# Performance work log

Hardware: AMD Instinct MI355X
Metric: run time of the kernel (lower is better)

## Reference

```python
import jax, jax.numpy as jnp
import numpy as np

DIM = 64        # feature channels of x
HEADS = 4
POS_DIM = 3
NUM_IDS = 8
STR_IN = 512    # strength_linear input size
B, S, W = 4, 1024, 8   # batch, sequence (S1), source-views (S2)


def setup_inputs() -> dict:
    key = jax.random.key(0)
    ks = jax.random.split(key, 18)
    stdv = 1.0 / np.sqrt(DIM * DIM)  # embedding init per module
    d8 = DIM // 8
    u = lambda k, shp, s: jax.random.uniform(k, shp, jnp.float32, -s, s)
    return {
        "x": jax.random.normal(ks[0], (B, DIM, S, W), jnp.float32),
        "pos": jax.random.normal(ks[1], (B, S, POS_DIM), jnp.float32),
        "strength": jax.random.normal(ks[2], (STR_IN,), jnp.float32),
        "embed_id1": 3,
        "q_emb_w": u(ks[3], (NUM_IDS, DIM * DIM), stdv),
        "k_emb_w": u(ks[4], (NUM_IDS, DIM * DIM), stdv),
        "v_emb_w": u(ks[5], (NUM_IDS, DIM * DIM), stdv),
        "pos_w1": u(ks[6], (POS_DIM, POS_DIM), 1.0 / np.sqrt(POS_DIM)),
        "pos_b1": u(ks[7], (POS_DIM,), 1.0 / np.sqrt(POS_DIM)),
        "pos_w2": u(ks[8], (d8, POS_DIM), 1.0 / np.sqrt(POS_DIM)),
        "pos_b2": u(ks[9], (d8,), 1.0 / np.sqrt(POS_DIM)),
        "head_w": u(ks[10], (HEADS, d8), 1.0 / np.sqrt(d8)),
        "head_b": u(ks[11], (HEADS,), 1.0 / np.sqrt(d8)),
        "gate": jnp.ones((HEADS,), jnp.float32),
        "out_w": u(ks[12], (DIM, DIM), 1.0 / np.sqrt(DIM)),
        "out_b": u(ks[13], (DIM,), 1.0 / np.sqrt(DIM)),
        "str_w": u(ks[14], (DIM, STR_IN), 1.0 / np.sqrt(STR_IN)),
        "str_b": u(ks[15], (DIM,), 1.0 / np.sqrt(STR_IN)),
    }


def reference(x, pos, strength, embed_id1, q_emb_w, k_emb_w, v_emb_w,
              pos_w1, pos_b1, pos_w2, pos_b2, head_w, head_b, gate,
              out_w, out_b, str_w, str_b):
    # strength projection: Linear(512, dim)
    s = strength @ str_w.T + str_b                    # [dim]
    xt = jnp.transpose(x, (0, 2, 3, 1))               # [B, S, W, dim]
    qe = q_emb_w[embed_id1].reshape(DIM, DIM)
    ke = k_emb_w[embed_id1].reshape(DIM, DIM)
    ve = v_emb_w[embed_id1].reshape(DIM, DIM)

    def proj(emb):
        y = xt @ emb.T + s                            # [B, S, W, dim]
        # collapse (W, dim) -> (heads, head_dim), heads to axis 1
        y = y.reshape(B, S, HEADS, -1)
        return jnp.transpose(y, (0, 2, 1, 3))         # [B, H, S, hd]

    q, k, v = proj(qe), proj(ke), proj(ve)
    hd = q.shape[-1]
    attn = jax.nn.softmax(jnp.einsum("bhsd,bhtd->bhst", q, k) / np.sqrt(hd), axis=-1)

    # relative-position attention branch
    ph = jax.nn.relu(pos @ pos_w1.T + pos_b1) @ pos_w2.T + pos_b2   # [B, S, dim//8]
    diff = ph[:, :, None, :] - ph[:, None, :, :]                    # [B, S, S, dim//8]
    pos_attn = jnp.transpose(diff @ head_w.T + head_b, (0, 3, 1, 2))
    pos_attn = jax.nn.softmax(pos_attn, axis=-1)                    # [B, H, S, S]

    g = jax.nn.sigmoid(gate).reshape(1, -1, 1, 1)
    attn = (1.0 - g) * attn + g * pos_attn
    attn = attn / jnp.sum(attn, axis=-1, keepdims=True)

    out = jnp.einsum("bhst,bhtd->bhsd", attn, v)      # [B, H, S, hd]
    out = jnp.transpose(out, (0, 2, 1, 3)).reshape(B, S, W, DIM)
    return out @ out_w.T + out_b                      # [B, S, W, dim]
```

## Files before the change

kernel.cpp:

```cpp
#include <hip/hip_runtime.h>
#include <math.h>
#include <stdint.h>

#define B_ 4
#define S_ 1024
#define F_ 512
#define HD 128
#define SOFT_C 4.0f

typedef __attribute__((ext_vector_type(8))) short short8;
typedef __attribute__((ext_vector_type(4))) float f32x4;
typedef __attribute__((ext_vector_type(4))) unsigned int u32x4;
typedef __attribute__((ext_vector_type(2))) unsigned int u32x2;

__device__ __forceinline__ unsigned short f2bf(float f) {
    unsigned int u = __float_as_uint(f);
    u = (u + 0x7FFFu + ((u >> 16) & 1u)) >> 16;
    return (unsigned short)u;
}
__device__ __forceinline__ float bf2f(unsigned int s) {
    return __uint_as_float(s << 16);
}
__device__ __forceinline__ void pack_hilo(const float* v, u32x4& hi, u32x4& lo) {
    #pragma unroll
    for (int p = 0; p < 4; ++p) {
        unsigned int h0 = f2bf(v[2 * p]), h1 = f2bf(v[2 * p + 1]);
        float l0 = v[2 * p] - bf2f(h0), l1 = v[2 * p + 1] - bf2f(h1);
        hi[p] = h0 | (h1 << 16);
        lo[p] = (unsigned int)f2bf(l0) | ((unsigned int)f2bf(l1) << 16);
    }
}

__global__ __launch_bounds__(256) void k_prep(
    const int* __restrict__ embed_id,
    const float* __restrict__ qw, const float* __restrict__ kw,
    const float* __restrict__ vw, const float* __restrict__ ow,
    const float* __restrict__ pos,
    const float* __restrict__ pw1, const float* __restrict__ pb1,
    const float* __restrict__ pw2, const float* __restrict__ pb2,
    const float* __restrict__ head_w,
    const float* __restrict__ strength, const float* __restrict__ str_w,
    const float* __restrict__ str_b,
    unsigned short* __restrict__ packs,
    float* __restrict__ sv, float* __restrict__ svq,
    float* __restrict__ p_g)
{
    __shared__ float red_s[4][4];
    __shared__ float inv_s[4];
    const int blk = blockIdx.x, tid = threadIdx.x;
    const float SCALE = 0.08838834764831845f;

    if (blk < 4) {
        const int id = embed_id[0];
        const float* src = (blk == 0 ? qw + id * 4096 : blk == 1 ? kw + id * 4096
                            : blk == 2 ? vw + id * 4096 : ow);
        const float scale = (blk == 0) ? SCALE : 1.0f;
        unsigned short* hi = packs + blk * 8192;
        unsigned short* lo = hi + 4096;
        for (int i = tid; i < 4096; i += 256) {
            float v = src[i] * scale;
            unsigned short h = f2bf(v);
            hi[i] = h;
            lo[i] = f2bf(v - bf2f(h));
        }
    } else if (blk < 8) {
        const int b = blk - 4;
        const int wv = tid >> 6;
        float w1_[9], b1_[3], w2_[24], b2_[8], hw_[32];
        #pragma unroll
        for (int i = 0; i < 9; ++i)  w1_[i] = pw1[i];
        #pragma unroll
        for (int i = 0; i < 3; ++i)  b1_[i] = pb1[i];
        #pragma unroll
        for (int i = 0; i < 24; ++i) w2_[i] = pw2[i];
        #pragma unroll
        for (int i = 0; i < 8; ++i)  b2_[i] = pb2[i];
        #pragma unroll
        for (int i = 0; i < 32; ++i) hw_[i] = head_w[i];

        float ev[4][4];
        float ps[4] = {0.f, 0.f, 0.f, 0.f};
        #pragma unroll
        for (int k = 0; k < 4; ++k) {
            const int t = k * 256 + tid;
            float p0 = pos[(b * S_ + t) * 3 + 0];
            float p1 = pos[(b * S_ + t) * 3 + 1];
            float p2 = pos[(b * S_ + t) * 3 + 2];
            float h0 = fmaxf(0.f, p0 * w1_[0] + p1 * w1_[1] + p2 * w1_[2] + b1_[0]);
            float h1 = fmaxf(0.f, p0 * w1_[3] + p1 * w1_[4] + p2 * w1_[5] + b1_[1]);
            float h2 = fmaxf(0.f, p0 * w1_[6] + p1 * w1_[7] + p2 * w1_[8] + b1_[2]);
            float ph[8];
            #pragma unroll
            for (int o8 = 0; o8 < 8; ++o8)
                ph[o8] = h0 * w2_[o8 * 3] + h1 * w2_[o8 * 3 + 1] + h2 * w2_[o8 * 3 + 2] + b2_[o8];
            #pragma unroll
            for (int h = 0; h < 4; ++h) {
                float A = 0.f;
                #pragma unroll
                for (int o8 = 0; o8 < 8; ++o8) A += ph[o8] * hw_[h * 8 + o8];
                ev[k][h] = __expf(-A - 1.0f);
                ps[h] += ev[k][h];
            }
        }
        #pragma unroll
        for (int h = 0; h < 4; ++h)
            #pragma unroll
            for (int off = 1; off < 64; off <<= 1)
                ps[h] += __shfl_xor(ps[h], off);
        if ((tid & 63) == 0)
            #pragma unroll
            for (int h = 0; h < 4; ++h) red_s[wv][h] = ps[h];
        __syncthreads();
        if (tid < 4)
            inv_s[tid] = 1.f / (red_s[0][tid] + red_s[1][tid] + red_s[2][tid] + red_s[3][tid]);
        __syncthreads();
        #pragma unroll
        for (int k = 0; k < 4; ++k)
            #pragma unroll
            for (int h = 0; h < 4; ++h)
                p_g[(b * 4 + h) * S_ + k * 256 + tid] = ev[k][h] * inv_s[h];
    } else {
        __shared__ float part_s[4][64];
        const int c = tid & 63, pr = tid >> 6;
        const float* wrow = str_w + c * 512 + pr * 128;
        const float* st   = strength + pr * 128;
        float acc = 0.f;
        #pragma unroll
        for (int j4 = 0; j4 < 32; ++j4) {
            f32x4 wv4 = *(const f32x4*)(wrow + j4 * 4);
            f32x4 s4  = *(const f32x4*)(st + j4 * 4);
            acc += wv4[0] * s4[0] + wv4[1] * s4[1] + wv4[2] * s4[2] + wv4[3] * s4[3];
        }
        part_s[pr][c] = acc;
        __syncthreads();
        if (tid < 64) {
            float v = part_s[0][tid] + part_s[1][tid] + part_s[2][tid]
                    + part_s[3][tid] + str_b[tid];
            sv[tid] = v;
            svq[tid] = v * SCALE;
        }
    }
}

__global__ __launch_bounds__(256) void k_qkv(
    const float* __restrict__ x,
    const unsigned short* __restrict__ packs,
    const float* __restrict__ sv, const float* __restrict__ svq,
    const float* __restrict__ p_g,
    unsigned short* __restrict__ yqh, unsigned short* __restrict__ ykh,
    unsigned short* __restrict__ yvt2, float* __restrict__ xbar)
{
    __shared__ float xr_s[4][8];
    const int tid  = threadIdx.x;
    const int wv   = tid >> 6;
    const int lane = tid & 63;
    const int quad = lane >> 4;
    const int l15  = lane & 15;

    if (blockIdx.x >= 512) {
        const int bi = blockIdx.x - 512;
        const int b = bi >> 6, c = bi & 63;
        const float* xc = x + (size_t)b * 524288 + c * 8192;
        const float* pb = p_g + b * 4096;
        float acc[8] = {};
        #pragma unroll
        for (int rr = 0; rr < 4; ++rr) {
            const int s = tid * 4 + rr;
            f32x4 x0 = *(const f32x4*)(xc + s * 8);
            f32x4 x1 = *(const f32x4*)(xc + s * 8 + 4);
            float p0 = pb[s], p1 = pb[1024 + s], p2 = pb[2048 + s], p3 = pb[3072 + s];
            acc[0] += p0 * x0[0]; acc[1] += p0 * x0[1];
            acc[2] += p1 * x0[2]; acc[3] += p1 * x0[3];
            acc[4] += p2 * x1[0]; acc[5] += p2 * x1[1];
            acc[6] += p3 * x1[2]; acc[7] += p3 * x1[3];
        }
        #pragma unroll
        for (int j = 0; j < 8; ++j)
            #pragma unroll
            for (int off = 1; off < 64; off <<= 1)
                acc[j] += __shfl_xor(acc[j], off);
        if (lane == 0)
            #pragma unroll
            for (int j = 0; j < 8; ++j) xr_s[wv][j] = acc[j];
        __syncthreads();
        if (tid < 8)
            xbar[(b * 8 + tid) * 64 + c] = xr_s[0][tid] + xr_s[1][tid]
                                         + xr_s[2][tid] + xr_s[3][tid];
        return;
    }

    const int r0   = blockIdx.x * 64 + wv * 16;
    const int b    = r0 >> 13;
    const int rloc = (r0 & 8191) + l15;
    const float* xb = x + (size_t)b * 524288;

    u32x4 xhi[2], xlo[2];
    #pragma unroll
    for (int kc = 0; kc < 2; ++kc) {
        float xv[8];
        #pragma unroll
        for (int j = 0; j < 8; ++j)
            xv[j] = xb[(kc * 32 + quad * 8 + j) * 8192 + rloc];
        pack_hilo(xv, xhi[kc], xlo[kc]);
    }

    float svq_l[4], sv_l[4];
    #pragma unroll
    for (int nt = 0; nt < 4; ++nt) {
        svq_l[nt] = svq[nt * 16 + l15];
        sv_l[nt]  = sv[nt * 16 + l15];
    }
    f32x4 svA[4];
    #pragma unroll
    for (int mt = 0; mt < 4; ++mt)
        svA[mt] = *(const f32x4*)(sv + mt * 16 + quad * 4);

    int idxq[4];
    #pragma unroll
    for (int rr = 0; rr < 4; ++rr) {
        const int rl = quad * 4 + rr;
        const int w_ = rl & 7;
        const int s_loc = ((r0 & 8191) >> 3) + (rl >> 3);
        idxq[rr] = (b * 4 + (w_ >> 1)) * 131072 + s_loc * 128 + (w_ & 1) * 64 + l15;
    }

    const int row_g = r0 + l15;
    const int s_idx = (row_g >> 3) & 1023;
    const int w_idx = row_g & 7;
    const int bh    = b * 4 + (w_idx >> 1);
    const int dbase = (w_idx & 1) * 64;
    unsigned short* vtb = yvt2 + (size_t)bh * 131072 + (s_idx >> 6) * 8192
                        + (size_t)dbase * 64 + (s_idx & 63);

    #pragma unroll
    for (int mat = 0; mat < 2; ++mat) {
        const unsigned short* mh = packs + mat * 8192;
        const unsigned short* ml = mh + 4096;
        f32x4 acc[4] = {};
        #pragma unroll
        for (int kc = 0; kc < 2; ++kc)
            #pragma unroll
            for (int nt = 0; nt < 4; ++nt) {
                const int off = (nt * 16 + l15) * 64 + kc * 32 + quad * 8;
                u32x4 ehi = *(const u32x4*)(mh + off);
                u32x4 elo = *(const u32x4*)(ml + off);
                acc[nt] = __builtin_amdgcn_mfma_f32_16x16x32_bf16(
                    __builtin_bit_cast(short8, xhi[kc]),
                    __builtin_bit_cast(short8, ehi), acc[nt], 0, 0, 0);
                acc[nt] = __builtin_amdgcn_mfma_f32_16x16x32_bf16(
                    __builtin_bit_cast(short8, xlo[kc]),
                    __builtin_bit_cast(short8, ehi), acc[nt], 0, 0, 0);
                acc[nt] = __builtin_amdgcn_mfma_f32_16x16x32_bf16(
                    __builtin_bit_cast(short8, xhi[kc]),
                    __builtin_bit_cast(short8, elo), acc[nt], 0, 0, 0);
            }
        unsigned short* y = (mat == 0 ? yqh : ykh);
        const float* svp = (mat == 0 ? svq_l : sv_l);
        #pragma unroll
        for (int nt = 0; nt < 4; ++nt)
            #pragma unroll
            for (int rr = 0; rr < 4; ++rr)
                y[(size_t)idxq[rr] + nt * 16] = f2bf(acc[nt][rr] + svp[nt]);
    }

    {
        const unsigned short* mh = packs + 2 * 8192;
        const unsigned short* ml = mh + 4096;
        f32x4 acc[4] = {};
        #pragma unroll
        for (int kc = 0; kc < 2; ++kc)
            #pragma unroll
            for (int mt = 0; mt < 4; ++mt) {
                const int off = (mt * 16 + l15) * 64 + kc * 32 + quad * 8;
                u32x4 ehi = *(const u32x4*)(mh + off);
                u32x4 elo = *(const u32x4*)(ml + off);
                acc[mt] = __builtin_amdgcn_mfma_f32_16x16x32_bf16(
                    __builtin_bit_cast(short8, ehi),
                    __builtin_bit_cast(short8, xhi[kc]), acc[mt], 0, 0, 0);
                acc[mt] = __builtin_amdgcn_mfma_f32_16x16x32_bf16(
                    __builtin_bit_cast(short8, ehi),
                    __builtin_bit_cast(short8, xlo[kc]), acc[mt], 0, 0, 0);
                acc[mt] = __builtin_amdgcn_mfma_f32_16x16x32_bf16(
                    __builtin_bit_cast(short8, elo),
                    __builtin_bit_cast(short8, xhi[kc]), acc[mt], 0, 0, 0);
            }
        #pragma unroll
        for (int mt = 0; mt < 4; ++mt)
            #pragma unroll
            for (int rr = 0; rr < 4; ++rr) {
                const int c = mt * 16 + quad * 4 + rr;
                vtb[(size_t)c * 64] = f2bf(acc[mt][rr] + svA[mt][rr]);
            }
    }
}

__global__ __launch_bounds__(256, 2) void k_attn(
    const unsigned short* __restrict__ yqh, const unsigned short* __restrict__ ykh,
    const unsigned short* __restrict__ yvt2,
    const float* __restrict__ xbar, const float* __restrict__ vw,
    const int* __restrict__ embed_id, const float* __restrict__ sv,
    const float* __restrict__ gate, float* __restrict__ out)
{
    __shared__ __align__(16) unsigned short kx[2][64 * 136];
    __shared__ __align__(16) unsigned short vx[2][128 * 72];
    __shared__ float vbar_s[128];

    const int tid  = threadIdx.x;
    const int w    = tid >> 6;
    const int lane = tid & 63;
    const int quad = lane >> 4;
    const int l15  = lane & 15;
    const int bh = blockIdx.x & 15, qt = blockIdx.x >> 4;
    const int b = bh >> 2, h = bh & 3;
    const int s0 = qt * 32;
    const int qh = w >> 1;
    const int dh = w & 1;

    const unsigned short* ykb = ykh + (size_t)bh * 131072;
    const unsigned short* yvb = yvt2 + (size_t)bh * 131072;

    if (tid < 128) {
        const int c = tid & 63, wloc = tid >> 6;
        const float* ver = vw + embed_id[0] * 4096 + c * 64;
        const float* xbr = xbar + (b * 8 + h * 2 + wloc) * 64;
        float a = sv[c];
        #pragma unroll
        for (int j4 = 0; j4 < 16; ++j4) {
            f32x4 e4 = *(const f32x4*)(ver + j4 * 4);
            f32x4 x4 = *(const f32x4*)(xbr + j4 * 4);
            a += e4[0] * x4[0] + e4[1] * x4[1] + e4[2] * x4[2] + e4[3] * x4[3];
        }
        vbar_s[wloc * 64 + c] = a;
    }

    u32x4 qf[4];
    #pragma unroll
    for (int kc = 0; kc < 4; ++kc)
        qf[kc] = *(const u32x4*)(yqh + (size_t)bh * 131072
                 + (s0 + qh * 16 + l15) * 128 + kc * 32 + quad * 8);

    #pragma unroll
    for (int r = 0; r < 4; ++r) {
        const int off = r * 2048 + tid * 8;
        *(u32x4*)&kx[0][(off >> 7) * 136 + (off & 127)] =
            *(const u32x4*)(ykb + off);
        *(u32x4*)&vx[0][(off >> 6) * 72 + (off & 63)] =
            *(const u32x4*)(yvb + off);
    }
    __syncthreads();

    f32x4 o[4] = {};
    float lsum = 0.f;
    const int srcA = ((quad & 1) << 5) + l15;

    for (int it = 0; it < 16; ++it) {
        const int cur = it & 1;
        u32x4 kst[4], vst[4];
        const bool pre = (it < 15);
        if (pre) {
            const unsigned short* ksrc = ykb + (it + 1) * 8192;
            const unsigned short* vsrc = yvb + (it + 1) * 8192;
            #pragma unroll
            for (int r = 0; r < 4; ++r)
                kst[r] = *(const u32x4*)(ksrc + r * 2048 + tid * 8);
            #pragma unroll
            for (int r = 0; r < 4; ++r)
                vst[r] = *(const u32x4*)(vsrc + r * 2048 + tid * 8);
        }

        const unsigned short* kxc = kx[cur];
        const unsigned short* vxc = vx[cur];

        #pragma unroll
        for (int th = 0; th < 2; ++th) {
            f32x4 sa0 = {}, sa1 = {};
            #pragma unroll
            for (int kc = 0; kc < 4; ++kc) {
                u32x4 a0 = *(const u32x4*)&kxc[(th * 32 + l15) * 136 + kc * 32 + quad * 8];
                sa0 = __builtin_amdgcn_mfma_f32_16x16x32_bf16(
                    __builtin_bit_cast(short8, a0),
                    __builtin_bit_cast(short8, qf[kc]), sa0, 0, 0, 0);
            }
            #pragma unroll
            for (int kc = 0; kc < 4; ++kc) {
                u32x4 a1 = *(const u32x4*)&kxc[(th * 32 + 16 + l15) * 136 + kc * 32 + quad * 8];
                sa1 = __builtin_amdgcn_mfma_f32_16x16x32_bf16(
                    __builtin_bit_cast(short8, a1),
                    __builtin_bit_cast(short8, qf[kc]), sa1, 0, 0, 0);
            }

            float p0[4], p1[4];
            #pragma unroll
            for (int r = 0; r < 4; ++r) {
                p0[r] = __expf(sa0[r] - SOFT_C);
                p1[r] = __expf(sa1[r] - SOFT_C);
                lsum += p0[r] + p1[r];
            }

            unsigned int pk00 = (unsigned int)f2bf(p0[0]) | ((unsigned int)f2bf(p0[1]) << 16);
            unsigned int pk01 = (unsigned int)f2bf(p0[2]) | ((unsigned int)f2bf(p0[3]) << 16);
            unsigned int pk10 = (unsigned int)f2bf(p1[0]) | ((unsigned int)f2bf(p1[1]) << 16);
            unsigned int pk11 = (unsigned int)f2bf(p1[2]) | ((unsigned int)f2bf(p1[3]) << 16);
            unsigned int sel0 = (quad < 2) ? pk00 : pk10;
            unsigned int sel1 = (quad < 2) ? pk01 : pk11;
            u32x4 pf;
            pf[0] = (unsigned int)__shfl((int)sel0, srcA);
            pf[1] = (unsigned int)__shfl((int)sel1, srcA);
            pf[2] = (unsigned int)__shfl((int)sel0, srcA + 16);
            pf[3] = (unsigned int)__shfl((int)sel1, srcA + 16);

            #pragma unroll
            for (int dt = 0; dt < 4; ++dt) {
                u32x4 vf = *(const u32x4*)&vxc[(dh * 64 + dt * 16 + l15) * 72
                                               + th * 32 + quad * 8];
                o[dt] = __builtin_amdgcn_mfma_f32_16x16x32_bf16(
                    __builtin_bit_cast(short8, vf),
                    __builtin_bit_cast(short8, pf), o[dt], 0, 0, 0);
            }
        }

        if (pre) {
            #pragma unroll
            for (int r = 0; r < 4; ++r) {
                const int off = r * 2048 + tid * 8;
                *(u32x4*)&kx[cur ^ 1][(off >> 7) * 136 + (off & 127)] = kst[r];
            }
            #pragma unroll
            for (int r = 0; r < 4; ++r) {
                const int off = r * 2048 + tid * 8;
                *(u32x4*)&vx[cur ^ 1][(off >> 6) * 72 + (off & 63)] = vst[r];
            }
        }
        __syncthreads();
    }

    lsum += __shfl_xor(lsum, 16);
    lsum += __shfl_xor(lsum, 32);
    const float gf = 1.f / (1.f + __expf(-gate[h]));
    const float cf = (1.f - gf) / lsum;
    const int row = b * S_ + s0 + qh * 16 + l15;
    #pragma unroll
    for (int dt = 0; dt < 4; ++dt) {
        const int d0 = dh * 64 + dt * 16 + quad * 4;
        f32x4 vb = *(const f32x4*)&vbar_s[d0];
        f32x4 rv;
        #pragma unroll
        for (int j = 0; j < 4; ++j) rv[j] = cf * o[dt][j] + gf * vb[j];
        *(f32x4*)(out + (size_t)row * F_ + h * HD + d0) = rv;
    }
}

__global__ __launch_bounds__(256) void k_oproj(
    float* __restrict__ out, const unsigned short* __restrict__ packs,
    const float* __restrict__ ob)
{
    const int tid  = threadIdx.x;
    const int wv   = tid >> 6;
    const int lane = tid & 63;
    const int quad = lane >> 4;
    const int l15  = lane & 15;
    const int r0   = blockIdx.x * 64 + wv * 16;
    const unsigned short* owh = packs + 3 * 8192;
    const unsigned short* owl = owh + 4096;

    u32x4 bhi[2], blo[2];
    #pragma unroll
    for (int kc = 0; kc < 2; ++kc) {
        const float* src = out + (size_t)(r0 + l15) * 64 + kc * 32 + quad * 8;
        f32x4 y0 = *(const f32x4*)src;
        f32x4 y1 = *(const f32x4*)(src + 4);
        float yv8[8] = {y0[0], y0[1], y0[2], y0[3], y1[0], y1[1], y1[2], y1[3]};
        pack_hilo(yv8, bhi[kc], blo[kc]);
    }

    f32x4 acc[4] = {};
    #pragma unroll
    for (int kc = 0; kc < 2; ++kc)
        #pragma unroll
        for (int mt = 0; mt < 4; ++mt) {
            const int off = (mt * 16 + l15) * 64 + kc * 32 + quad * 8;
            u32x4 ahi = *(const u32x4*)(owh + off);
            u32x4 alo = *(const u32x4*)(owl + off);
            acc[mt] = __builtin_amdgcn_mfma_f32_16x16x32_bf16(
                __builtin_bit_cast(short8, ahi),
                __builtin_bit_cast(short8, bhi[kc]), acc[mt], 0, 0, 0);
            acc[mt] = __builtin_amdgcn_mfma_f32_16x16x32_bf16(
                __builtin_bit_cast(short8, ahi),
                __builtin_bit_cast(short8, blo[kc]), acc[mt], 0, 0, 0);
            acc[mt] = __builtin_amdgcn_mfma_f32_16x16x32_bf16(
                __builtin_bit_cast(short8, alo),
                __builtin_bit_cast(short8, bhi[kc]), acc[mt], 0, 0, 0);
        }

    #pragma unroll
    for (int mt = 0; mt < 4; ++mt) {
        f32x4 bias = *(const f32x4*)(ob + mt * 16 + quad * 4);
        f32x4 v = acc[mt] + bias;
        *(f32x4*)(out + (size_t)(r0 + l15) * 64 + mt * 16 + quad * 4) = v;
    }
}

extern "C" void kernel_launch(void* const* d_in, const int* in_sizes, int n_in,
                              void* d_out, int out_size, void* d_ws, size_t ws_size,
                              hipStream_t stream) {
    (void)in_sizes; (void)n_in; (void)out_size; (void)ws_size;
    const float* x        = (const float*)d_in[0];
    const float* pos      = (const float*)d_in[1];
    const float* strength = (const float*)d_in[2];
    const int*   embed_id = (const int*)d_in[3];
    const float* qw       = (const float*)d_in[4];
    const float* kw       = (const float*)d_in[5];
    const float* vw       = (const float*)d_in[6];
    const float* pw1      = (const float*)d_in[7];
    const float* pb1      = (const float*)d_in[8];
    const float* pw2      = (const float*)d_in[9];
    const float* pb2      = (const float*)d_in[10];
    const float* head_w   = (const float*)d_in[11];
    const float* gate     = (const float*)d_in[13];
    const float* out_w    = (const float*)d_in[14];
    const float* out_b    = (const float*)d_in[15];
    const float* str_w    = (const float*)d_in[16];
    const float* str_b    = (const float*)d_in[17];
    float* out = (float*)d_out;

    unsigned short* yqh   = (unsigned short*)d_ws;
    unsigned short* ykh   = yqh + 2097152;
    unsigned short* yvt2  = ykh + 2097152;
    unsigned short* packs = yvt2 + 2097152;
    float* sv   = (float*)(packs + 8 * 4096);
    float* svq  = sv + 64;
    float* p_g  = svq + 64;
    float* xbar = p_g + 16384;

    k_prep<<<9, 256, 0, stream>>>(embed_id, qw, kw, vw, out_w, pos,
                                  pw1, pb1, pw2, pb2, head_w,
                                  strength, str_w, str_b, packs, sv, svq, p_g);
    k_qkv<<<768, 256, 0, stream>>>(x, packs, sv, svq, p_g, yqh, ykh, yvt2, xbar);
    k_attn<<<512, 256, 0, stream>>>(yqh, ykh, yvt2, xbar, vw, embed_id, sv,
                                    gate, out);
    k_oproj<<<512, 256, 0, stream>>>(out, packs, out_b);
}
```

Before: 159.9 us.

## Fuse prep into QKV kernel and output projection into attention epilogue

The separate prep kernel is removed. Each QKV block now recomputes the strength projection and the hi/lo bf16 split of the Q/K/V weights into shared memory, in a swizzled layout. The xbar blocks recompute the position softmax themselves. The output-projection kernel is folded into the attention epilogue: partial outputs are reduced through shared memory, projected with out_w split on the fly, and the gated vbar term is pre-projected. The intent is to remove two launches and a global round trip of the attention output, at the cost of redundant per-block weight conversion and larger shared memory use that may lower occupancy.

```diff
diff --git a/kernel.cpp b/kernel.cpp
--- a/kernel.cpp
+++ b/kernel.cpp
@@ -31,148 +31,103 @@
     }
 }
 
-__global__ __launch_bounds__(256) void k_prep(
-    const int* __restrict__ embed_id,
+__global__ __launch_bounds__(256) void k_qkv(
+    const float* __restrict__ x, const int* __restrict__ embed_id,
     const float* __restrict__ qw, const float* __restrict__ kw,
-    const float* __restrict__ vw, const float* __restrict__ ow,
-    const float* __restrict__ pos,
-    const float* __restrict__ pw1, const float* __restrict__ pb1,
-    const float* __restrict__ pw2, const float* __restrict__ pb2,
-    const float* __restrict__ head_w,
+    const float* __restrict__ vw,
     const float* __restrict__ strength, const float* __restrict__ str_w,
     const float* __restrict__ str_b,
-    unsigned short* __restrict__ packs,
-    float* __restrict__ sv, float* __restrict__ svq,
-    float* __restrict__ p_g)
+    const float* __restrict__ pos, const float* __restrict__ pw1,
+    const float* __restrict__ pb1, const float* __restrict__ pw2,
+    const float* __restrict__ pb2, const float* __restrict__ head_w,
+    unsigned short* __restrict__ yqh, unsigned short* __restrict__ ykh,
+    unsigned short* __restrict__ yvt2,
+    float* __restrict__ sv_g, float* __restrict__ xbar)
 {
+    __shared__ unsigned short whi[3][4096];
+    __shared__ unsigned short wlo[3][4096];
+    __shared__ float part_s[4][64];
+    __shared__ float sv_s[64], svq_s[64];
+    __shared__ float xr_s[4][8];
     __shared__ float red_s[4][4];
     __shared__ float inv_s[4];
-    const int blk = blockIdx.x, tid = threadIdx.x;
-    const float SCALE = 0.08838834764831845f;
-
-    if (blk < 4) {
-        const int id = embed_id[0];
-        const float* src = (blk == 0 ? qw + id * 4096 : blk == 1 ? kw + id * 4096
-                            : blk == 2 ? vw + id * 4096 : ow);
-        const float scale = (blk == 0) ? SCALE : 1.0f;
-        unsigned short* hi = packs + blk * 8192;
-        unsigned short* lo = hi + 4096;
-        for (int i = tid; i < 4096; i += 256) {
-            float v = src[i] * scale;
-            unsigned short h = f2bf(v);
-            hi[i] = h;
-            lo[i] = f2bf(v - bf2f(h));
-        }
-    } else if (blk < 8) {
-        const int b = blk - 4;
-        const int wv = tid >> 6;
-        float w1_[9], b1_[3], w2_[24], b2_[8], hw_[32];
-        #pragma unroll
-        for (int i = 0; i < 9; ++i)  w1_[i] = pw1[i];
-        #pragma unroll
-        for (int i = 0; i < 3; ++i)  b1_[i] = pb1[i];
-        #pragma unroll
-        for (int i = 0; i < 24; ++i) w2_[i] = pw2[i];
-        #pragma unroll
-        for (int i = 0; i < 8; ++i)  b2_[i] = pb2[i];
-        #pragma unroll
-        for (int i = 0; i < 32; ++i) hw_[i] = head_w[i];
-
-        float ev[4][4];
-        float ps[4] = {0.f, 0.f, 0.f, 0.f};
-        #pragma unroll
-        for (int k = 0; k < 4; ++k) {
-            const int t = k * 256 + tid;
-            float p0 = pos[(b * S_ + t) * 3 + 0];
-            float p1 = pos[(b * S_ + t) * 3 + 1];
-            float p2 = pos[(b * S_ + t) * 3 + 2];
-            float h0 = fmaxf(0.f, p0 * w1_[0] + p1 * w1_[1] + p2 * w1_[2] + b1_[0]);
-            float h1 = fmaxf(0.f, p0 * w1_[3] + p1 * w1_[4] + p2 * w1_[5] + b1_[1]);
-            float h2 = fmaxf(0.f, p0 * w1_[6] + p1 * w1_[7] + p2 * w1_[8] + b1_[2]);
-            float ph[8];
-            #pragma unroll
-            for (int o8 = 0; o8 < 8; ++o8)
-                ph[o8] = h0 * w2_[o8 * 3] + h1 * w2_[o8 * 3 + 1] + h2 * w2_[o8 * 3 + 2] + b2_[o8];
-            #pragma unroll
-            for (int h = 0; h < 4; ++h) {
-                float A = 0.f;
-                #pragma unroll
-                for (int o8 = 0; o8 < 8; ++o8) A += ph[o8] * hw_[h * 8 + o8];
-                ev[k][h] = __expf(-A - 1.0f);
-                ps[h] += ev[k][h];
-            }
-        }
-        #pragma unroll
-        for (int h = 0; h < 4; ++h)
-            #pragma unroll
-            for (int off = 1; off < 64; off <<= 1)
-                ps[h] += __shfl_xor(ps[h], off);
-        if ((tid & 63) == 0)
-            #pragma unroll
-            for (int h = 0; h < 4; ++h) red_s[wv][h] = ps[h];
-        __syncthreads();
-        if (tid < 4)
-            inv_s[tid] = 1.f / (red_s[0][tid] + red_s[1][tid] + red_s[2][tid] + red_s[3][tid]);
-        __syncthreads();
-        #pragma unroll
-        for (int k = 0; k < 4; ++k)
-            #pragma unroll
-            for (int h = 0; h < 4; ++h)
-                p_g[(b * 4 + h) * S_ + k * 256 + tid] = ev[k][h] * inv_s[h];
-    } else {
-        __shared__ float part_s[4][64];
-        const int c = tid & 63, pr = tid >> 6;
-        const float* wrow = str_w + c * 512 + pr * 128;
-        const float* st   = strength + pr * 128;
-        float acc = 0.f;
-        #pragma unroll
-        for (int j4 = 0; j4 < 32; ++j4) {
-            f32x4 wv4 = *(const f32x4*)(wrow + j4 * 4);
-            f32x4 s4  = *(const f32x4*)(st + j4 * 4);
-            acc += wv4[0] * s4[0] + wv4[1] * s4[1] + wv4[2] * s4[2] + wv4[3] * s4[3];
-        }
-        part_s[pr][c] = acc;
-        __syncthreads();
-        if (tid < 64) {
-            float v = part_s[0][tid] + part_s[1][tid] + part_s[2][tid]
-                    + part_s[3][tid] + str_b[tid];
-            sv[tid] = v;
-            svq[tid] = v * SCALE;
-        }
-    }
-}
-
-__global__ __launch_bounds__(256) void k_qkv(
-    const float* __restrict__ x,
-    const unsigned short* __restrict__ packs,
-    const float* __restrict__ sv, const float* __restrict__ svq,
-    const float* __restrict__ p_g,
-    unsigned short* __restrict__ yqh, unsigned short* __restrict__ ykh,
-    unsigned short* __restrict__ yvt2, float* __restrict__ xbar)
-{
-    __shared__ float xr_s[4][8];
+
     const int tid  = threadIdx.x;
     const int wv   = tid >> 6;
     const int lane = tid & 63;
     const int quad = lane >> 4;
     const int l15  = lane & 15;
+    const float SCALE = 0.08838834764831845f;
 
     if (blockIdx.x >= 512) {
         const int bi = blockIdx.x - 512;
         const int b = bi >> 6, c = bi & 63;
+        float w1_[9], b1_[3], w2_[24], b2_[8], hw_[32];
+        #pragma unroll
+        for (int i = 0; i < 9; ++i)  w1_[i] = pw1[i];
+        #pragma unroll
+        for (int i = 0; i < 3; ++i)  b1_[i] = pb1[i];
+        #pragma unroll
+        for (int i = 0; i < 24; ++i) w2_[i] = pw2[i];
+        #pragma unroll
+        for (int i = 0; i < 8; ++i)  b2_[i] = pb2[i];
+        #pragma unroll
+        for (int i = 0; i < 32; ++i) hw_[i] = head_w[i];
+
+        float pv_[4][4];
+        float ps[4] = {0.f, 0.f, 0.f, 0.f};
+        #pragma unroll
+        for (int rr = 0; rr < 4; ++rr) {
+            const int s = tid * 4 + rr;
+            float p0 = pos[(b * S_ + s) * 3 + 0];
+            float p1 = pos[(b * S_ + s) * 3 + 1];
+            float p2 = pos[(b * S_ + s) * 3 + 2];
+            float h0 = fmaxf(0.f, p0 * w1_[0] + p1 * w1_[1] + p2 * w1_[2] + b1_[0]);
+            float h1 = fmaxf(0.f, p0 * w1_[3] + p1 * w1_[4] + p2 * w1_[5] + b1_[1]);
+            float h2 = fmaxf(0.f, p0 * w1_[6] + p1 * w1_[7] + p2 * w1_[8] + b1_[2]);
+            float ph[8];
+            #pragma unroll
+            for (int o8 = 0; o8 < 8; ++o8)
+                ph[o8] = h0 * w2_[o8 * 3] + h1 * w2_[o8 * 3 + 1]
+                       + h2 * w2_[o8 * 3 + 2] + b2_[o8];
+            #pragma unroll
+            for (int h = 0; h < 4; ++h) {
+                float A = 0.f;
+                #pragma unroll
+                for (int o8 = 0; o8 < 8; ++o8) A += ph[o8] * hw_[h * 8 + o8];
+                pv_[rr][h] = __expf(-A - 1.0f);
+                ps[h] += pv_[rr][h];
+            }
+        }
+        #pragma unroll
+        for (int h = 0; h < 4; ++h)
+            #pragma unroll
+            for (int off = 1; off < 64; off <<= 1)
+                ps[h] += __shfl_xor(ps[h], off);
+        if (lane == 0)
+            #pragma unroll
+            for (int h = 0; h < 4; ++h) red_s[wv][h] = ps[h];
+        __syncthreads();
+        if (tid < 4)
+            inv_s[tid] = 1.f / (red_s[0][tid] + red_s[1][tid]
+                              + red_s[2][tid] + red_s[3][tid]);
+        __syncthreads();
+
         const float* xc = x + (size_t)b * 524288 + c * 8192;
-        const float* pb = p_g + b * 4096;
         float acc[8] = {};
         #pragma unroll
         for (int rr = 0; rr < 4; ++rr) {
             const int s = tid * 4 + rr;
             f32x4 x0 = *(const f32x4*)(xc + s * 8);
             f32x4 x1 = *(const f32x4*)(xc + s * 8 + 4);
-            float p0 = pb[s], p1 = pb[1024 + s], p2 = pb[2048 + s], p3 = pb[3072 + s];
-            acc[0] += p0 * x0[0]; acc[1] += p0 * x0[1];
-            acc[2] += p1 * x0[2]; acc[3] += p1 * x0[3];
-            acc[4] += p2 * x1[0]; acc[5] += p2 * x1[1];
-            acc[6] += p3 * x1[2]; acc[7] += p3 * x1[3];
+            float q0 = pv_[rr][0] * inv_s[0];
+            float q1 = pv_[rr][1] * inv_s[1];
+            float q2 = pv_[rr][2] * inv_s[2];
+            float q3 = pv_[rr][3] * inv_s[3];
+            acc[0] += q0 * x0[0]; acc[1] += q0 * x0[1];
+            acc[2] += q1 * x0[2]; acc[3] += q1 * x0[3];
+            acc[4] += q2 * x1[0]; acc[5] += q2 * x1[1];
+            acc[6] += q3 * x1[2]; acc[7] += q3 * x1[3];
         }
         #pragma unroll
         for (int j = 0; j < 8; ++j)
@@ -189,6 +144,43 @@
         return;
     }
 
+    const int id = embed_id[0];
+    #pragma unroll
+    for (int m = 0; m < 3; ++m) {
+        const float* src = (m == 0 ? qw : m == 1 ? kw : vw) + id * 4096;
+        const float sc = (m == 0) ? SCALE : 1.0f;
+        for (int i = tid; i < 4096; i += 256) {
+            float v = src[i] * sc;
+            unsigned short hh = f2bf(v);
+            const int r = i >> 6, cc = i & 63;
+            const int off = ((r >> 4) * 2 + (cc >> 5)) * 512
+                          + ((cc >> 3) & 3) * 128 + (r & 15) * 8 + (cc & 7);
+            whi[m][off] = hh;
+            wlo[m][off] = f2bf(v - bf2f(hh));
+        }
+    }
+    {
+        const float* wrow = str_w + lane * 512 + wv * 128;
+        const float* st   = strength + wv * 128;
+        float a = 0.f;
+        #pragma unroll
+        for (int j4 = 0; j4 < 32; ++j4) {
+            f32x4 wv4 = *(const f32x4*)(wrow + j4 * 4);
+            f32x4 s4  = *(const f32x4*)(st + j4 * 4);
+            a += wv4[0] * s4[0] + wv4[1] * s4[1] + wv4[2] * s4[2] + wv4[3] * s4[3];
+        }
+        part_s[wv][lane] = a;
+    }
+    __syncthreads();
+    if (tid < 64) {
+        float v = part_s[0][tid] + part_s[1][tid] + part_s[2][tid]
+                + part_s[3][tid] + str_b[tid];
+        sv_s[tid]  = v;
+        svq_s[tid] = v * SCALE;
+        if (blockIdx.x == 0) sv_g[tid] = v;
+    }
+    __syncthreads();
+
     const int r0   = blockIdx.x * 64 + wv * 16;
     const int b    = r0 >> 13;
     const int rloc = (r0 & 8191) + l15;
@@ -207,13 +199,13 @@
     float svq_l[4], sv_l[4];
     #pragma unroll
     for (int nt = 0; nt < 4; ++nt) {
-        svq_l[nt] = svq[nt * 16 + l15];
-        sv_l[nt]  = sv[nt * 16 + l15];
+        svq_l[nt] = svq_s[nt * 16 + l15];
+        sv_l[nt]  = sv_s[nt * 16 + l15];
     }
     f32x4 svA[4];
     #pragma unroll
     for (int mt = 0; mt < 4; ++mt)
-        svA[mt] = *(const f32x4*)(sv + mt * 16 + quad * 4);
+        svA[mt] = *(const f32x4*)&sv_s[mt * 16 + quad * 4];
 
     int idxq[4];
     #pragma unroll
@@ -234,14 +226,14 @@
 
     #pragma unroll
     for (int mat = 0; mat < 2; ++mat) {
-        const unsigned short* mh = packs + mat * 8192;
-        const unsigned short* ml = mh + 4096;
+        const unsigned short* mh = whi[mat];
+        const unsigned short* ml = wlo[mat];
         f32x4 acc[4] = {};
         #pragma unroll
         for (int kc = 0; kc < 2; ++kc)
             #pragma unroll
             for (int nt = 0; nt < 4; ++nt) {
-                const int off = (nt * 16 + l15) * 64 + kc * 32 + quad * 8;
+                const int off = (nt * 2 + kc) * 512 + quad * 128 + l15 * 8;
                 u32x4 ehi = *(const u32x4*)(mh + off);
                 u32x4 elo = *(const u32x4*)(ml + off);
                 acc[nt] = __builtin_amdgcn_mfma_f32_16x16x32_bf16(
@@ -264,14 +256,14 @@
     }
 
     {
-        const unsigned short* mh = packs + 2 * 8192;
-        const unsigned short* ml = mh + 4096;
+        const unsigned short* mh = whi[2];
+        const unsigned short* ml = wlo[2];
         f32x4 acc[4] = {};
         #pragma unroll
         for (int kc = 0; kc < 2; ++kc)
             #pragma unroll
             for (int mt = 0; mt < 4; ++mt) {
-                const int off = (mt * 16 + l15) * 64 + kc * 32 + quad * 8;
+                const int off = (mt * 2 + kc) * 512 + quad * 128 + l15 * 8;
                 u32x4 ehi = *(const u32x4*)(mh + off);
                 u32x4 elo = *(const u32x4*)(ml + off);
                 acc[mt] = __builtin_amdgcn_mfma_f32_16x16x32_bf16(
@@ -299,11 +291,15 @@
     const unsigned short* __restrict__ yvt2,
     const float* __restrict__ xbar, const float* __restrict__ vw,
     const int* __restrict__ embed_id, const float* __restrict__ sv,
-    const float* __restrict__ gate, float* __restrict__ out)
+    const float* __restrict__ gate,
+    const float* __restrict__ out_w, const float* __restrict__ out_b,
+    float* __restrict__ out)
 {
     __shared__ __align__(16) unsigned short kx[2][64 * 136];
     __shared__ __align__(16) unsigned short vx[2][128 * 72];
     __shared__ float vbar_s[128];
+    __shared__ float vbarP_s[128];
+    __shared__ float lsq_s[2][2][16];
 
     const int tid  = threadIdx.x;
     const int w    = tid >> 6;
@@ -314,7 +310,7 @@
     const int b = bh >> 2, h = bh & 3;
     const int s0 = qt * 32;
     const int qh = w >> 1;
-    const int dh = w & 1;
+    const int ts = w & 1;
 
     const unsigned short* ykb = ykh + (size_t)bh * 131072;
     const unsigned short* yvb = yvt2 + (size_t)bh * 131072;
@@ -349,7 +345,20 @@
     }
     __syncthreads();
 
-    f32x4 o[4] = {};
+    if (tid < 128) {
+        const int seg = tid >> 6, dq = tid & 63;
+        const float* wr = out_w + dq * 64;
+        float a = 0.f;
+        #pragma unroll
+        for (int j4 = 0; j4 < 16; ++j4) {
+            f32x4 w4 = *(const f32x4*)(wr + j4 * 4);
+            f32x4 v4 = *(const f32x4*)&vbar_s[seg * 64 + j4 * 4];
+            a += w4[0] * v4[0] + w4[1] * v4[1] + w4[2] * v4[2] + w4[3] * v4[3];
+        }
+        vbarP_s[seg * 64 + dq] = a;
+    }
+
+    f32x4 o[8] = {};
     float lsum = 0.f;
     const int srcA = ((quad & 1) << 5) + l15;
 
@@ -371,52 +380,48 @@
         const unsigned short* kxc = kx[cur];
         const unsigned short* vxc = vx[cur];
 
-        #pragma unroll
-        for (int th = 0; th < 2; ++th) {
-            f32x4 sa0 = {}, sa1 = {};
-            #pragma unroll
-            for (int kc = 0; kc < 4; ++kc) {
-                u32x4 a0 = *(const u32x4*)&kxc[(th * 32 + l15) * 136 + kc * 32 + quad * 8];
-                sa0 = __builtin_amdgcn_mfma_f32_16x16x32_bf16(
-                    __builtin_bit_cast(short8, a0),
-                    __builtin_bit_cast(short8, qf[kc]), sa0, 0, 0, 0);
-            }
-            #pragma unroll
-            for (int kc = 0; kc < 4; ++kc) {
-                u32x4 a1 = *(const u32x4*)&kxc[(th * 32 + 16 + l15) * 136 + kc * 32 + quad * 8];
-                sa1 = __builtin_amdgcn_mfma_f32_16x16x32_bf16(
-                    __builtin_bit_cast(short8, a1),
-                    __builtin_bit_cast(short8, qf[kc]), sa1, 0, 0, 0);
-            }
-
-            float p0[4], p1[4];
-            #pragma unroll
-            for (int r = 0; r < 4; ++r) {
-                p0[r] = __expf(sa0[r] - SOFT_C);
-                p1[r] = __expf(sa1[r] - SOFT_C);
-                lsum += p0[r] + p1[r];
-            }
-
-            unsigned int pk00 = (unsigned int)f2bf(p0[0]) | ((unsigned int)f2bf(p0[1]) << 16);
-            unsigned int pk01 = (unsigned int)f2bf(p0[2]) | ((unsigned int)f2bf(p0[3]) << 16);
-            unsigned int pk10 = (unsigned int)f2bf(p1[0]) | ((unsigned int)f2bf(p1[1]) << 16);
-            unsigned int pk11 = (unsigned int)f2bf(p1[2]) | ((unsigned int)f2bf(p1[3]) << 16);
-            unsigned int sel0 = (quad < 2) ? pk00 : pk10;
-            unsigned int sel1 = (quad < 2) ? pk01 : pk11;
-            u32x4 pf;
-            pf[0] = (unsigned int)__shfl((int)sel0, srcA);
-            pf[1] = (unsigned int)__shfl((int)sel1, srcA);
-            pf[2] = (unsigned int)__shfl((int)sel0, srcA + 16);
-            pf[3] = (unsigned int)__shfl((int)sel1, srcA + 16);
-
-            #pragma unroll
-            for (int dt = 0; dt < 4; ++dt) {
-                u32x4 vf = *(const u32x4*)&vxc[(dh * 64 + dt * 16 + l15) * 72
-                                               + th * 32 + quad * 8];
-                o[dt] = __builtin_amdgcn_mfma_f32_16x16x32_bf16(
-                    __builtin_bit_cast(short8, vf),
-                    __builtin_bit_cast(short8, pf), o[dt], 0, 0, 0);
-            }
+        f32x4 sa0 = {}, sa1 = {};
+        #pragma unroll
+        for (int kc = 0; kc < 4; ++kc) {
+            u32x4 a0 = *(const u32x4*)&kxc[(ts * 32 + l15) * 136 + kc * 32 + quad * 8];
+            sa0 = __builtin_amdgcn_mfma_f32_16x16x32_bf16(
+                __builtin_bit_cast(short8, a0),
+                __builtin_bit_cast(short8, qf[kc]), sa0, 0, 0, 0);
+        }
+        #pragma unroll
+        for (int kc = 0; kc < 4; ++kc) {
+            u32x4 a1 = *(const u32x4*)&kxc[(ts * 32 + 16 + l15) * 136 + kc * 32 + quad * 8];
+            sa1 = __builtin_amdgcn_mfma_f32_16x16x32_bf16(
+                __builtin_bit_cast(short8, a1),
+                __builtin_bit_cast(short8, qf[kc]), sa1, 0, 0, 0);
+        }
+
+        float p0[4], p1[4];
+        #pragma unroll
+        for (int r = 0; r < 4; ++r) {
+            p0[r] = __expf(sa0[r] - SOFT_C);
+            p1[r] = __expf(sa1[r] - SOFT_C);
+            lsum += p0[r] + p1[r];
+        }
+
+        unsigned int pk00 = (unsigned int)f2bf(p0[0]) | ((unsigned int)f2bf(p0[1]) << 16);
+        unsigned int pk01 = (unsigned int)f2bf(p0[2]) | ((unsigned int)f2bf(p0[3]) << 16);
+        unsigned int pk10 = (unsigned int)f2bf(p1[0]) | ((unsigned int)f2bf(p1[1]) << 16);
+        unsigned int pk11 = (unsigned int)f2bf(p1[2]) | ((unsigned int)f2bf(p1[3]) << 16);
+        unsigned int sel0 = (quad < 2) ? pk00 : pk10;
+        unsigned int sel1 = (quad < 2) ? pk01 : pk11;
+        u32x4 pf;
+        pf[0] = (unsigned int)__shfl((int)sel0, srcA);
+        pf[1] = (unsigned int)__shfl((int)sel1, srcA);
+        pf[2] = (unsigned int)__shfl((int)sel0, srcA + 16);
+        pf[3] = (unsigned int)__shfl((int)sel1, srcA + 16);
+
+        #pragma unroll
+        for (int dt = 0; dt < 8; ++dt) {
+            u32x4 vf = *(const u32x4*)&vxc[(dt * 16 + l15) * 72 + ts * 32 + quad * 8];
+            o[dt] = __builtin_amdgcn_mfma_f32_16x16x32_bf16(
+                __builtin_bit_cast(short8, vf),
+                __builtin_bit_cast(short8, pf), o[dt], 0, 0, 0);
         }
 
         if (pre) {
@@ -434,43 +439,36 @@
         __syncthreads();
     }
 
+    float* obuf = (float*)&kx[0][0];
+    {
+        float* ow_ = obuf + ((qh * 2 + ts) * 16 + l15) * 132;
+        #pragma unroll
+        for (int dt = 0; dt < 8; ++dt)
+            *(f32x4*)(ow_ + dt * 16 + quad * 4) = o[dt];
+    }
     lsum += __shfl_xor(lsum, 16);
     lsum += __shfl_xor(lsum, 32);
+    if (quad == 0) lsq_s[qh][ts][l15] = lsum;
+    __syncthreads();
+
     const float gf = 1.f / (1.f + __expf(-gate[h]));
-    const float cf = (1.f - gf) / lsum;
-    const int row = b * S_ + s0 + qh * 16 + l15;
-    #pragma unroll
-    for (int dt = 0; dt < 4; ++dt) {
-        const int d0 = dh * 64 + dt * 16 + quad * 4;
-        f32x4 vb = *(const f32x4*)&vbar_s[d0];
-        f32x4 rv;
-        #pragma unroll
-        for (int j = 0; j < 4; ++j) rv[j] = cf * o[dt][j] + gf * vb[j];
-        *(f32x4*)(out + (size_t)row * F_ + h * HD + d0) = rv;
-    }
-}
-
-__global__ __launch_bounds__(256) void k_oproj(
-    float* __restrict__ out, const unsigned short* __restrict__ packs,
-    const float* __restrict__ ob)
-{
-    const int tid  = threadIdx.x;
-    const int wv   = tid >> 6;
-    const int lane = tid & 63;
-    const int quad = lane >> 4;
-    const int l15  = lane & 15;
-    const int r0   = blockIdx.x * 64 + wv * 16;
-    const unsigned short* owh = packs + 3 * 8192;
-    const unsigned short* owl = owh + 4096;
+    const float cf = (1.f - gf) / (lsq_s[qh][0][l15] + lsq_s[qh][1][l15]);
+    const float* oa  = obuf + ((qh * 2 + 0) * 16 + l15) * 132;
+    const float* obp = obuf + ((qh * 2 + 1) * 16 + l15) * 132;
 
     u32x4 bhi[2], blo[2];
     #pragma unroll
     for (int kc = 0; kc < 2; ++kc) {
-        const float* src = out + (size_t)(r0 + l15) * 64 + kc * 32 + quad * 8;
-        f32x4 y0 = *(const f32x4*)src;
-        f32x4 y1 = *(const f32x4*)(src + 4);
-        float yv8[8] = {y0[0], y0[1], y0[2], y0[3], y1[0], y1[1], y1[2], y1[3]};
-        pack_hilo(yv8, bhi[kc], blo[kc]);
+        const int off = ts * 64 + kc * 32 + quad * 8;
+        f32x4 a0 = *(const f32x4*)(oa + off);
+        f32x4 a1 = *(const f32x4*)(oa + off + 4);
+        f32x4 c0 = *(const f32x4*)(obp + off);
+        f32x4 c1 = *(const f32x4*)(obp + off + 4);
+        float yv[8] = {cf * (a0[0] + c0[0]), cf * (a0[1] + c0[1]),
+                       cf * (a0[2] + c0[2]), cf * (a0[3] + c0[3]),
+                       cf * (a1[0] + c1[0]), cf * (a1[1] + c1[1]),
+                       cf * (a1[2] + c1[2]), cf * (a1[3] + c1[3])};
+        pack_hilo(yv, bhi[kc], blo[kc]);
     }
 
     f32x4 acc[4] = {};
@@ -478,9 +476,12 @@
     for (int kc = 0; kc < 2; ++kc)
         #pragma unroll
         for (int mt = 0; mt < 4; ++mt) {
-            const int off = (mt * 16 + l15) * 64 + kc * 32 + quad * 8;
-            u32x4 ahi = *(const u32x4*)(owh + off);
-            u32x4 alo = *(const u32x4*)(owl + off);
+            const float* wsrc2 = out_w + (mt * 16 + l15) * 64 + kc * 32 + quad * 8;
+            f32x4 w0 = *(const f32x4*)wsrc2;
+            f32x4 w1 = *(const f32x4*)(wsrc2 + 4);
+            float wv8[8] = {w0[0], w0[1], w0[2], w0[3], w1[0], w1[1], w1[2], w1[3]};
+            u32x4 ahi, alo;
+            pack_hilo(wv8, ahi, alo);
             acc[mt] = __builtin_amdgcn_mfma_f32_16x16x32_bf16(
                 __builtin_bit_cast(short8, ahi),
                 __builtin_bit_cast(short8, bhi[kc]), acc[mt], 0, 0, 0);
@@ -492,11 +493,16 @@
                 __builtin_bit_cast(short8, bhi[kc]), acc[mt], 0, 0, 0);
         }
 
+    const int w_seg = h * 2 + ts;
+    const size_t rowb = ((size_t)(b * S_ + s0 + qh * 16 + l15) * 8 + w_seg) * 64;
     #pragma unroll
     for (int mt = 0; mt < 4; ++mt) {
-        f32x4 bias = *(const f32x4*)(ob + mt * 16 + quad * 4);
-        f32x4 v = acc[mt] + bias;
-        *(f32x4*)(out + (size_t)(r0 + l15) * 64 + mt * 16 + quad * 4) = v;
+        f32x4 vb   = *(const f32x4*)&vbarP_s[ts * 64 + mt * 16 + quad * 4];
+        f32x4 bias = *(const f32x4*)(out_b + mt * 16 + quad * 4);
+        f32x4 res;
+        #pragma unroll
+        for (int j = 0; j < 4; ++j) res[j] = acc[mt][j] + gf * vb[j] + bias[j];
+        *(f32x4*)(out + rowb + mt * 16 + quad * 4) = res;
     }
 }
 
@@ -526,17 +532,13 @@
     unsigned short* yqh   = (unsigned short*)d_ws;
     unsigned short* ykh   = yqh + 2097152;
     unsigned short* yvt2  = ykh + 2097152;
-    unsigned short* packs = yvt2 + 2097152;
-    float* sv   = (float*)(packs + 8 * 4096);
-    float* svq  = sv + 64;
-    float* p_g  = svq + 64;
-    float* xbar = p_g + 16384;
-
-    k_prep<<<9, 256, 0, stream>>>(embed_id, qw, kw, vw, out_w, pos,
-                                  pw1, pb1, pw2, pb2, head_w,
-                                  strength, str_w, str_b, packs, sv, svq, p_g);
-    k_qkv<<<768, 256, 0, stream>>>(x, packs, sv, svq, p_g, yqh, ykh, yvt2, xbar);
+    float* sv   = (float*)(yvt2 + 2097152);
+    float* xbar = sv + 64;
+
+    k_qkv<<<768, 256, 0, stream>>>(x, embed_id, qw, kw, vw,
+                                   strength, str_w, str_b,
+                                   pos, pw1, pb1, pw2, pb2, head_w,
+                                   yqh, ykh, yvt2, sv, xbar);
     k_attn<<<512, 256, 0, stream>>>(yqh, ykh, yvt2, xbar, vw, embed_id, sv,
-                                    gate, out);
-    k_oproj<<<512, 256, 0, stream>>>(out, packs, out_b);
+                                    gate, out_w, out_b, out);
 }
```

After: 144.0 us. 1.11x faster.
